# Optimization experiments

Hardware: AMD Instinct MI355X
Metric: run time of the kernel (lower is better)

Reference implementation:

```python
import jax, jax.numpy as jnp
import numpy as np
import math

EPS = 1.1920929e-07  # torch F.rms_norm default eps = fp32 machine epsilon


def rms_norm(x):
    # normalize over last dim, no learned weight (matches F.rms_norm(x, (d,)))
    var = jnp.mean(jnp.square(x), axis=-1, keepdims=True)
    return x * jax.lax.rsqrt(var + EPS)


def rotary(x, cos, sin):
    # x: (B, T, H, D); cos/sin: (T, D) -> broadcast over B, H
    d2 = x.shape[-1] // 2
    x1, x2 = x[..., :d2], x[..., d2:]
    rot = jnp.concatenate([-x2, x1], axis=-1)  # rotate_half
    c = cos[None, :, None, :]
    s = sin[None, :, None, :]
    return x * c + rot * s


def setup_inputs() -> dict:
    key = jax.random.key(0)
    ks = jax.random.split(key, 5)
    B, T, C, H = 2, 2048, 1024, 16
    D = C // H
    x = jax.random.normal(ks[0], (B, T, C), dtype=jnp.float32)
    # real RoPE tables (theta=10000), duplicated across the two halves
    inv_freq = 1.0 / (10000.0 ** (np.arange(0, D, 2, dtype=np.float32) / D))
    pos = np.arange(T, dtype=np.float32)
    freqs = np.outer(pos, inv_freq)            # (T, D/2)
    emb = np.concatenate([freqs, freqs], -1)   # (T, D)
    cos = jnp.asarray(np.cos(emb), dtype=jnp.float32)
    sin = jnp.asarray(np.sin(emb), dtype=jnp.float32)
    sc_in = 1.0 / math.sqrt(C)
    W_attn = jax.random.normal(ks[1], (C, 3 * C), dtype=jnp.float32) * sc_in
    b_attn = jax.random.normal(ks[2], (3 * C,), dtype=jnp.float32) * 0.02
    W_proj = jax.random.normal(ks[3], (C, C), dtype=jnp.float32) * sc_in
    b_proj = jax.random.normal(ks[4], (C,), dtype=jnp.float32) * 0.02
    return {"x": x, "cos": cos, "sin": sin, "W_attn": W_attn, "b_attn": b_attn,
            "W_proj": W_proj, "b_proj": b_proj}


def reference(x, cos, sin, W_attn, b_attn, W_proj, b_proj):
    B, T, C = x.shape
    H = 16
    D = C // H
    qkv = x @ W_attn + b_attn                         # (B, T, 3C)
    qkv = qkv.reshape(B, T, 3, H, D)                  # 'b t (a h d) -> ...'
    q, k, v = qkv[:, :, 0], qkv[:, :, 1], qkv[:, :, 2]  # (B, T, H, D)
    q, k = rms_norm(q), rms_norm(k)
    q = rotary(q, cos, sin)
    k = rotary(k, cos, sin)
    # causal SDPA, scale = 1/sqrt(D)
    scale = 1.0 / math.sqrt(D)
    scores = jnp.einsum('bthd,bshd->bhts', q, k) * scale  # (B, H, T, T)
    causal = jnp.tril(jnp.ones((T, T), dtype=bool))
    scores = jnp.where(causal[None, None], scores, jnp.finfo(scores.dtype).min)
    attn = jax.nn.softmax(scores, axis=-1)
    y = jnp.einsum('bhts,bshd->bthd', attn, v)            # (B, T, H, D)
    y = y.reshape(B, T, C)
    return y @ W_proj + b_proj
```

## Files before the change

kernel.cpp:

```cpp
#include <hip/hip_runtime.h>
#include <math.h>

#define EPSV 1.1920929e-07f

typedef __attribute__((ext_vector_type(8))) short short8;
typedef __attribute__((ext_vector_type(4))) float f32x4;

__device__ __forceinline__ float bf2f(unsigned short u) {
    union { unsigned int i; float f; } c; c.i = ((unsigned int)u) << 16; return c.f;
}
__device__ __forceinline__ unsigned short f2bf(float f) {
    union { float f; unsigned int i; } c; c.f = f;
    unsigned int r = c.i + 0x7FFFu + ((c.i >> 16) & 1u);
    return (unsigned short)(r >> 16);
}
__device__ __forceinline__ unsigned int pack_bf16_ru(float a, float b) {
    union { float f; unsigned int i; } ca, cb; ca.f = a; cb.f = b;
    return __builtin_amdgcn_perm(cb.i + 0x8000u, ca.i + 0x8000u, 0x07060302u);
}
__device__ __forceinline__ void async_lds16(const unsigned short* g, unsigned short* l) {
    __builtin_amdgcn_global_load_lds(
        (const __attribute__((address_space(1))) unsigned int*)g,
        (__attribute__((address_space(3))) unsigned int*)l, 16, 0, 0);
}

__global__ __launch_bounds__(256) void prep_cast_transpose(
    const float* __restrict__ x, unsigned short* __restrict__ xb, int nCast,
    const float* __restrict__ Wa, unsigned short* __restrict__ Wat,
    const float* __restrict__ Wp, unsigned short* __restrict__ Wpt,
    int castBlocks)
{
    __shared__ float tile[32][33];
    const int bxg = blockIdx.x;
    if (bxg < castBlocks) {
        const int i = (bxg * 256 + threadIdx.x) * 4;
        if (i >= nCast) return;
        const float4 v = *(const float4*)&x[i];
        ushort4 o;
        o.x = f2bf(v.x); o.y = f2bf(v.y); o.z = f2bf(v.z); o.w = f2bf(v.w);
        *(ushort4*)&xb[i] = o;
        return;
    }
    const int r0 = bxg - castBlocks;
    int bx = r0 & 127;
    const int by = r0 >> 7;
    const float* W; unsigned short* Wt; int N;
    if (bx < 96) { W = Wa; Wt = Wat; N = 3072; }
    else         { W = Wp; Wt = Wpt; N = 1024; bx -= 96; }
    const int n0 = bx * 32, k0 = by * 32;
    const int r = threadIdx.x >> 3, c4 = (threadIdx.x & 7) * 4;
    const float4 v = *(const float4*)&W[(size_t)(k0 + r) * N + n0 + c4];
    tile[r][c4 + 0] = v.x; tile[r][c4 + 1] = v.y;
    tile[r][c4 + 2] = v.z; tile[r][c4 + 3] = v.w;
    __syncthreads();
    ushort4 o;
    o.x = f2bf(tile[c4 + 0][r]); o.y = f2bf(tile[c4 + 1][r]);
    o.z = f2bf(tile[c4 + 2][r]); o.w = f2bf(tile[c4 + 3][r]);
    *(ushort4*)&Wt[(size_t)(n0 + r) * 1024 + k0 + c4] = o;
}

template <bool OUT_BF16>
__global__ __launch_bounds__(256) void gemm_bf16(
    const unsigned short* __restrict__ A,
    const unsigned short* __restrict__ Bt,
    const float* __restrict__ bias,
    void* __restrict__ Cv,
    int M, int N, int K)
{
    __shared__ unsigned short As0[128][32], As1[128][32];
    __shared__ unsigned short Bs0[128][32], Bs1[128][32];
    const int t    = threadIdx.x;
    const int lane = t & 63;
    const int wv   = t >> 6;
    const int wrow = (wv >> 1) * 64;
    const int wcol = (wv & 1) * 64;
    const int m0 = blockIdx.y * 128;
    const int n0 = blockIdx.x * 128;
    const int col  = lane & 15;
    const int quad = lane >> 4;

    const int srow = (wv << 5) + (lane >> 2);
    const int scol = (lane & 3) << 3;
    const unsigned short* a00 = A  + (size_t)(m0 + srow) * K + scol;
    const unsigned short* a10 = a00 + (size_t)16 * K;
    const unsigned short* a01 = a00 + 32;
    const unsigned short* a11 = a10 + 32;
    const unsigned short* b00 = Bt + (size_t)(n0 + srow) * K + scol;
    const unsigned short* b10 = b00 + (size_t)16 * K;
    const unsigned short* b01 = b00 + 32;
    const unsigned short* b11 = b10 + 32;
    unsigned short* al0 = &As0[srow][scol];
    unsigned short* al1 = &As0[srow + 16][scol];
    unsigned short* al2 = &As1[srow][scol];
    unsigned short* al3 = &As1[srow + 16][scol];
    unsigned short* bl0 = &Bs0[srow][scol];
    unsigned short* bl1 = &Bs0[srow + 16][scol];
    unsigned short* bl2 = &Bs1[srow][scol];
    unsigned short* bl3 = &Bs1[srow + 16][scol];

    f32x4 acc[4][4];
    #pragma unroll
    for (int i = 0; i < 4; ++i)
        #pragma unroll
        for (int j = 0; j < 4; ++j)
            acc[i][j] = (f32x4){0.f, 0.f, 0.f, 0.f};

    for (int k0 = 0; k0 < K; k0 += 64) {
        async_lds16(a00, al0);
        async_lds16(a10, al1);
        async_lds16(a01, al2);
        async_lds16(a11, al3);
        async_lds16(b00, bl0);
        async_lds16(b10, bl1);
        async_lds16(b01, bl2);
        async_lds16(b11, bl3);
        a00 += 64; a10 += 64; a01 += 64; a11 += 64;
        b00 += 64; b10 += 64; b01 += 64; b11 += 64;
        __syncthreads();
        short8 af[2][4], bf[2][4];
        #pragma unroll
        for (int mt = 0; mt < 4; ++mt) {
            af[0][mt] = *(const short8*)&As0[wrow + mt * 16 + col][quad << 3];
            af[1][mt] = *(const short8*)&As1[wrow + mt * 16 + col][quad << 3];
        }
        #pragma unroll
        for (int nt = 0; nt < 4; ++nt) {
            bf[0][nt] = *(const short8*)&Bs0[wcol + nt * 16 + col][quad << 3];
            bf[1][nt] = *(const short8*)&Bs1[wcol + nt * 16 + col][quad << 3];
        }
        #pragma unroll
        for (int ks = 0; ks < 2; ++ks)
            #pragma unroll
            for (int mt = 0; mt < 4; ++mt)
                #pragma unroll
                for (int nt = 0; nt < 4; ++nt)
                    acc[mt][nt] = __builtin_amdgcn_mfma_f32_16x16x32_bf16(
                        af[ks][mt], bf[ks][nt], acc[mt][nt], 0, 0, 0);
        __syncthreads();
    }

    const int rowq = quad << 2;
    #pragma unroll
    for (int nt = 0; nt < 4; ++nt) {
        const int n = n0 + wcol + nt * 16 + col;
        const float bv = bias[n];
        #pragma unroll
        for (int mt = 0; mt < 4; ++mt) {
            #pragma unroll
            for (int r = 0; r < 4; ++r) {
                const int m = m0 + wrow + mt * 16 + rowq + r;
                const float v = acc[mt][nt][r] + bv;
                if (OUT_BF16)
                    ((unsigned short*)Cv)[(size_t)m * N + n] = f2bf(v);
                else
                    ((float*)Cv)[(size_t)m * N + n] = v;
            }
        }
    }
}

__global__ __launch_bounds__(256) void gemm_bf16_n64(
    const unsigned short* __restrict__ A,
    const unsigned short* __restrict__ Bt,
    const float* __restrict__ bias,
    float* __restrict__ C,
    int M, int N, int K)
{
    __shared__ unsigned short As0[128][32], As1[128][32];
    __shared__ unsigned short Bs0[64][32], Bs1[64][32];
    const int t    = threadIdx.x;
    const int lane = t & 63;
    const int wv   = t >> 6;
    const int wrow = wv << 5;
    const int m0 = blockIdx.y * 128;
    const int n0 = blockIdx.x * 64;
    const int col  = lane & 15;
    const int quad = lane >> 4;

    const int srow = (wv << 5) + (lane >> 2);
    const int scol = (lane & 3) << 3;
    const unsigned short* a00 = A  + (size_t)(m0 + srow) * K + scol;
    const unsigned short* a10 = a00 + (size_t)16 * K;
    const unsigned short* a01 = a00 + 32;
    const unsigned short* a11 = a10 + 32;
    const int bsrow = (wv << 4) + (lane >> 2);
    const unsigned short* b00 = Bt + (size_t)(n0 + bsrow) * K + scol;
    const unsigned short* b01 = b00 + 32;
    unsigned short* al0 = &As0[srow][scol];
    unsigned short* al1 = &As0[srow + 16][scol];
    unsigned short* al2 = &As1[srow][scol];
    unsigned short* al3 = &As1[srow + 16][scol];
    unsigned short* bl0 = &Bs0[bsrow][scol];
    unsigned short* bl1 = &Bs1[bsrow][scol];

    f32x4 acc[2][4];
    #pragma unroll
    for (int i = 0; i < 2; ++i)
        #pragma unroll
        for (int j = 0; j < 4; ++j)
            acc[i][j] = (f32x4){0.f, 0.f, 0.f, 0.f};

    for (int k0 = 0; k0 < K; k0 += 64) {
        async_lds16(a00, al0);
        async_lds16(a10, al1);
        async_lds16(a01, al2);
        async_lds16(a11, al3);
        async_lds16(b00, bl0);
        async_lds16(b01, bl1);
        a00 += 64; a10 += 64; a01 += 64; a11 += 64;
        b00 += 64; b01 += 64;
        __syncthreads();
        short8 af[2][2], bf[2][4];
        #pragma unroll
        for (int mt = 0; mt < 2; ++mt) {
            af[0][mt] = *(const short8*)&As0[wrow + mt * 16 + col][quad << 3];
            af[1][mt] = *(const short8*)&As1[wrow + mt * 16 + col][quad << 3];
        }
        #pragma unroll
        for (int nt = 0; nt < 4; ++nt) {
            bf[0][nt] = *(const short8*)&Bs0[nt * 16 + col][quad << 3];
            bf[1][nt] = *(const short8*)&Bs1[nt * 16 + col][quad << 3];
        }
        #pragma unroll
        for (int ks = 0; ks < 2; ++ks)
            #pragma unroll
            for (int mt = 0; mt < 2; ++mt)
                #pragma unroll
                for (int nt = 0; nt < 4; ++nt)
                    acc[mt][nt] = __builtin_amdgcn_mfma_f32_16x16x32_bf16(
                        af[ks][mt], bf[ks][nt], acc[mt][nt], 0, 0, 0);
        __syncthreads();
    }

    const int rowq = quad << 2;
    #pragma unroll
    for (int nt = 0; nt < 4; ++nt) {
        const int n = n0 + nt * 16 + col;
        const float bv = bias[n];
        #pragma unroll
        for (int mt = 0; mt < 2; ++mt) {
            #pragma unroll
            for (int r = 0; r < 4; ++r) {
                const int m = m0 + wrow + mt * 16 + rowq + r;
                C[(size_t)m * N + n] = acc[mt][nt][r] + bv;
            }
        }
    }
}

__global__ __launch_bounds__(256) void rmsrope_vt(
    unsigned short* __restrict__ qkv, const float* __restrict__ cosp,
    const float* __restrict__ sinp, unsigned short* __restrict__ vt,
    int BT, int T)
{
    __shared__ unsigned short tile[64][72];
    const int nrms = BT * 2;
    const int bxg = (int)blockIdx.x;
    if (bxg < nrms) {
        const int wid  = (bxg << 2) + (threadIdx.x >> 6);
        const int lane = threadIdx.x & 63;
        const int hq = wid & 3;
        const int w  = (wid >> 2) & 1;
        const int bt = wid >> 3;
        if (bt >= BT) return;
        const int h  = (hq << 2) + (lane >> 4);
        const int d4 = (lane & 15) << 2;
        const int tpos = bt % T;
        const size_t idx = (size_t)bt * 3072 + (w << 10) + (h << 6) + d4;

        const ushort4 u = *(const ushort4*)&qkv[idx];
        const float x0 = bf2f(u.x), x1 = bf2f(u.y), x2 = bf2f(u.z), x3 = bf2f(u.w);
        float ss = x0 * x0 + x1 * x1 + x2 * x2 + x3 * x3;
        ss += __shfl_xor(ss, 1, 64);
        ss += __shfl_xor(ss, 2, 64);
        ss += __shfl_xor(ss, 4, 64);
        ss += __shfl_xor(ss, 8, 64);
        const float rn = rsqrtf(ss * (1.0f / 64.0f) + EPSV);
        const float xn0 = x0 * rn, xn1 = x1 * rn, xn2 = x2 * rn, xn3 = x3 * rn;
        const float p0 = __shfl_xor(xn0, 8, 64);
        const float p1 = __shfl_xor(xn1, 8, 64);
        const float p2 = __shfl_xor(xn2, 8, 64);
        const float p3 = __shfl_xor(xn3, 8, 64);
        const float sgn = (d4 < 32) ? -1.0f : 1.0f;
        const float4 c = *(const float4*)&cosp[tpos * 64 + d4];
        const float4 s = *(const float4*)&sinp[tpos * 64 + d4];
        const float scale = (w == 0) ? 0.18033688011112042f : 1.0f;
        ushort4 o;
        o.x = f2bf(fmaf(xn0, c.x, sgn * p0 * s.x) * scale);
        o.y = f2bf(fmaf(xn1, c.y, sgn * p1 * s.y) * scale);
        o.z = f2bf(fmaf(xn2, c.z, sgn * p2 * s.z) * scale);
        o.w = f2bf(fmaf(xn3, c.w, sgn * p3 * s.w) * scale);
        *(ushort4*)&qkv[idx] = o;
        return;
    }
    const int r0 = bxg - nrms;
    const int tdiv = T >> 6;
    const int bh = r0 / tdiv;
    const int ty = r0 - bh * tdiv;
    const int b  = bh >> 4, h = bh & 15;
    const int t0 = ty << 6;
    const int t  = threadIdx.x;
    const unsigned short* vbase = qkv + (size_t)b * T * 3072 + 2048 + (h << 6);

    #pragma unroll
    for (int i = 0; i < 2; ++i) {
        const int c = t + (i << 8);
        const int r = c >> 3, c8 = (c & 7) << 3;
        const short8 v = *(const short8*)&vbase[(size_t)(t0 + r) * 3072 + c8];
        #pragma unroll
        for (int j = 0; j < 8; ++j)
            tile[c8 + j][r] = (unsigned short)v[j];
    }
    __syncthreads();
    #pragma unroll
    for (int i = 0; i < 2; ++i) {
        const int c = t + (i << 8);
        const int d = c >> 3, c8 = (c & 7) << 3;
        const short8 o = *(const short8*)&tile[d][c8];
        *(short8*)&vt[((size_t)bh * 64 + d) * T + t0 + c8] = o;
    }
}

__global__ __launch_bounds__(512, 4) void flash_attn_mfma(
    const unsigned short* __restrict__ qkv,
    const unsigned short* __restrict__ vt,
    unsigned short* __restrict__ yb,
    int B, int T)
{
    const int bh = blockIdx.x;
    const int b  = bh >> 4, h = bh & 15;
    const int ny = (int)gridDim.y;
    const int y  = (int)blockIdx.y;
    const int hny = (ny + 1) >> 1;
    const int jq = (y < hny) ? (ny - 1 - y) : (y - hny);
    const int q0 = jq << 7;
    const int t  = threadIdx.x;
    const int lane = t & 63;
    const int w    = t >> 6;
    const int col  = lane & 15;
    const int quad = lane >> 4;

    __shared__ __align__(16) unsigned short smem[25600];
    unsigned short* Kb = smem;
    unsigned short* Vb = smem + 8192;
    unsigned short* Ps = smem + 16384;

    const unsigned short* qb  = qkv + (size_t)b * T * 3072 + (h << 6);
    const unsigned short* kb  = qb + 1024;
    const unsigned short* vtb = vt + (size_t)bh * 64 * T;

    const int qw = q0 + (w << 4);
    const int qg = qw + col;

    short8 qf[2];
    {
        const unsigned short* qrow = qb + (size_t)qg * 3072 + (quad << 3);
        qf[0] = *(const short8*)&qrow[0];
        qf[1] = *(const short8*)&qrow[32];
    }

    f32x4 oacc[4];
    #pragma unroll
    for (int i = 0; i < 4; ++i) oacc[i] = (f32x4){0.f, 0.f, 0.f, 0.f};
    float l_i = 0.f;

    const int sr = t >> 3;
    const int sg = (((t & 7) ^ (sr & 7)) << 3);
    const unsigned short* kp = kb  + (size_t)sr * 3072 + sg;
    const unsigned short* vp = vtb + (size_t)sr * T + sg;

    async_lds16(kp, Kb + (t << 3));
    async_lds16(vp, Vb + (t << 3));
    kp += (size_t)64 * 3072; vp += 64;

    const int cs0 = ((quad ^ (col & 7)) << 3);
    const int cs1 = (((4 + quad) ^ (col & 7)) << 3);

    const int last_kt = (q0 + 127) >> 6;
    int cur = 0;
    for (int kt = 0; kt <= last_kt; ++kt) {
        const int k0 = kt << 6;
        __syncthreads();
        if (kt < last_kt) {
            async_lds16(kp, Kb + ((cur ^ 1) << 12) + (t << 3));
            async_lds16(vp, Vb + ((cur ^ 1) << 12) + (t << 3));
            kp += (size_t)64 * 3072; vp += 64;
        }

        if (k0 <= qw + 15) {
            const unsigned short* Kc = Kb + (cur << 12);
            const unsigned short* Vc = Vb + (cur << 12);

            f32x4 st[4];
            #pragma unroll
            for (int i = 0; i < 4; ++i) st[i] = (f32x4){0.f, 0.f, 0.f, 0.f};
            __builtin_amdgcn_s_setprio(1);
            #pragma unroll
            for (int ks = 0; ks < 2; ++ks)
                #pragma unroll
                for (int mt = 0; mt < 4; ++mt) {
                    const short8 kf = *(const short8*)&Kc[(mt * 16 + col) * 64 + (ks ? cs1 : cs0)];
                    st[mt] = __builtin_amdgcn_mfma_f32_16x16x32_bf16(kf, qf[ks], st[mt], 0, 0, 0);
                }
            __builtin_amdgcn_s_setprio(0);

            const bool diag = (k0 + 63 > qw);
            unsigned short* pw = Ps + ((w << 4) + col) * 72;
            float rs = 0.f;
            #pragma unroll
            for (int mt = 0; mt < 4; ++mt) {
                float x0 = st[mt][0], x1 = st[mt][1];
                float x2 = st[mt][2], x3 = st[mt][3];
                if (diag) {
                    const int sbase = k0 + mt * 16 + (quad << 2);
                    if (sbase + 0 > qg) x0 = -INFINITY;
                    if (sbase + 1 > qg) x1 = -INFINITY;
                    if (sbase + 2 > qg) x2 = -INFINITY;
                    if (sbase + 3 > qg) x3 = -INFINITY;
                }
                const float p0 = __builtin_amdgcn_exp2f(x0);
                const float p1 = __builtin_amdgcn_exp2f(x1);
                const float p2 = __builtin_amdgcn_exp2f(x2);
                const float p3 = __builtin_amdgcn_exp2f(x3);
                rs += (p0 + p1) + (p2 + p3);
                uint2 pk;
                pk.x = pack_bf16_ru(p0, p1);
                pk.y = pack_bf16_ru(p2, p3);
                *(uint2*)&pw[mt * 16 + (quad << 2)] = pk;
            }
            l_i += rs;

            __builtin_amdgcn_s_setprio(1);
            #pragma unroll
            for (int ks = 0; ks < 2; ++ks) {
                const short8 pf = *(const short8*)&Ps[((w << 4) + col) * 72 + ks * 32 + (quad << 3)];
                #pragma unroll
                for (int mt = 0; mt < 4; ++mt) {
                    const short8 vf = *(const short8*)&Vc[(mt * 16 + col) * 64 + (ks ? cs1 : cs0)];
                    oacc[mt] = __builtin_amdgcn_mfma_f32_16x16x32_bf16(vf, pf, oacc[mt], 0, 0, 0);
                }
            }
            __builtin_amdgcn_s_setprio(0);
        }
        cur ^= 1;
    }

    l_i += __shfl_xor(l_i, 16, 64);
    l_i += __shfl_xor(l_i, 32, 64);
    const float inv = 1.0f / l_i;
    unsigned short* yrow = yb + (size_t)(b * T + qg) * 1024 + (h << 6);
    #pragma unroll
    for (int mt = 0; mt < 4; ++mt) {
        ushort4 yv;
        yv.x = f2bf(oacc[mt][0] * inv);
        yv.y = f2bf(oacc[mt][1] * inv);
        yv.z = f2bf(oacc[mt][2] * inv);
        yv.w = f2bf(oacc[mt][3] * inv);
        *(ushort4*)&yrow[mt * 16 + (quad << 2)] = yv;
    }
}

extern "C" void kernel_launch(void* const* d_in, const int* in_sizes, int n_in,
                              void* d_out, int out_size, void* d_ws, size_t ws_size,
                              hipStream_t stream)
{
    const float* x      = (const float*)d_in[0];
    const float* cosp   = (const float*)d_in[1];
    const float* sinp   = (const float*)d_in[2];
    const float* W_attn = (const float*)d_in[3];
    const float* b_attn = (const float*)d_in[4];
    const float* W_proj = (const float*)d_in[5];
    const float* b_proj = (const float*)d_in[6];
    float* out = (float*)d_out;

    const int C = 1024, H = 16;
    const int T  = in_sizes[1] / 64;
    const int BT = in_sizes[0] / C;
    const int B  = BT / T;

    unsigned short* qkvb = (unsigned short*)d_ws;
    unsigned short* xb   = qkvb + (size_t)BT * 3072;
    unsigned short* Wab  = xb   + (size_t)BT * 1024;
    unsigned short* Wpb  = Wab  + (size_t)3072 * 1024;
    unsigned short* yb   = Wpb  + (size_t)1024 * 1024;
    unsigned short* vtb  = xb;

    const int castBlocks = BT * C / 1024;
    prep_cast_transpose<<<dim3(castBlocks + 4096), dim3(256), 0, stream>>>(
        x, xb, BT * C, W_attn, Wab, W_proj, Wpb, castBlocks);

    gemm_bf16<true><<<dim3(3 * C / 128, BT / 128), dim3(256), 0, stream>>>(
        xb, Wab, b_attn, qkvb, BT, 3 * C, C);

    rmsrope_vt<<<dim3(BT * 2 + B * H * (T >> 6)), dim3(256), 0, stream>>>(
        qkvb, cosp, sinp, vtb, BT, T);

    flash_attn_mfma<<<dim3(B * H, T / 128), dim3(512), 0, stream>>>(
        qkvb, vtb, yb, B, T);

    gemm_bf16_n64<<<dim3(C / 64, BT / 128), dim3(256), 0, stream>>>(
        yb, Wpb, b_proj, out, BT, C, C);
}
```

Measured before the change: 186.2 us.

## Fuse RMSNorm, RoPE and V transpose into QKV GEMM epilogue

Removes the separate rmsrope_vt kernel. The QKV GEMM epilogue now computes the per-head RMS norm with wave shuffles, applies rotary using a packed cos/sin table built in the prep kernel, and writes V transposed through LDS. This removes one launch and a full bf16 round trip of q/k/v through global memory. In exchange the epilogue uses strided 2-byte stores, holds more registers, and adds an extra workspace buffer for vt.

```diff
diff --git a/kernel.cpp b/kernel.cpp
--- a/kernel.cpp
+++ b/kernel.cpp
@@ -28,7 +28,8 @@
     const float* __restrict__ x, unsigned short* __restrict__ xb, int nCast,
     const float* __restrict__ Wa, unsigned short* __restrict__ Wat,
     const float* __restrict__ Wp, unsigned short* __restrict__ Wpt,
-    int castBlocks)
+    const float* __restrict__ cosp, const float* __restrict__ sinp,
+    float2* __restrict__ cs, int castBlocks)
 {
     __shared__ float tile[32][33];
     const int bxg = blockIdx.x;
@@ -39,6 +40,12 @@
         ushort4 o;
         o.x = f2bf(v.x); o.y = f2bf(v.y); o.z = f2bf(v.z); o.w = f2bf(v.w);
         *(ushort4*)&xb[i] = o;
+        return;
+    }
+    if (bxg >= castBlocks + 4096) {
+        const int i = (bxg - castBlocks - 4096) * 256 + threadIdx.x;
+        const int tp = i >> 5, dp = i & 31;
+        cs[i] = make_float2(cosp[tp * 64 + dp], sinp[tp * 64 + dp]);
         return;
     }
     const int r0 = bxg - castBlocks;
@@ -59,16 +66,22 @@
     *(ushort4*)&Wt[(size_t)(n0 + r) * 1024 + k0 + c4] = o;
 }
 
-template <bool OUT_BF16>
-__global__ __launch_bounds__(256) void gemm_bf16(
+__global__ __launch_bounds__(256) void gemm_qkv(
     const unsigned short* __restrict__ A,
     const unsigned short* __restrict__ Bt,
     const float* __restrict__ bias,
-    void* __restrict__ Cv,
-    int M, int N, int K)
+    unsigned short* __restrict__ qkv,
+    unsigned short* __restrict__ vt,
+    const float2* __restrict__ cs,
+    int M, int K, int T)
 {
-    __shared__ unsigned short As0[128][32], As1[128][32];
-    __shared__ unsigned short Bs0[128][32], Bs1[128][32];
+    const int N = 3072;
+    __shared__ __align__(16) unsigned short smem[17408];
+    unsigned short* As0 = smem;
+    unsigned short* As1 = smem + 4096;
+    unsigned short* Bs0 = smem + 8192;
+    unsigned short* Bs1 = smem + 12288;
+
     const int t    = threadIdx.x;
     const int lane = t & 63;
     const int wv   = t >> 6;
@@ -89,14 +102,14 @@
     const unsigned short* b10 = b00 + (size_t)16 * K;
     const unsigned short* b01 = b00 + 32;
     const unsigned short* b11 = b10 + 32;
-    unsigned short* al0 = &As0[srow][scol];
-    unsigned short* al1 = &As0[srow + 16][scol];
-    unsigned short* al2 = &As1[srow][scol];
-    unsigned short* al3 = &As1[srow + 16][scol];
-    unsigned short* bl0 = &Bs0[srow][scol];
-    unsigned short* bl1 = &Bs0[srow + 16][scol];
-    unsigned short* bl2 = &Bs1[srow][scol];
-    unsigned short* bl3 = &Bs1[srow + 16][scol];
+    unsigned short* al0 = &As0[srow * 32 + scol];
+    unsigned short* al1 = &As0[(srow + 16) * 32 + scol];
+    unsigned short* al2 = &As1[srow * 32 + scol];
+    unsigned short* al3 = &As1[(srow + 16) * 32 + scol];
+    unsigned short* bl0 = &Bs0[srow * 32 + scol];
+    unsigned short* bl1 = &Bs0[(srow + 16) * 32 + scol];
+    unsigned short* bl2 = &Bs1[srow * 32 + scol];
+    unsigned short* bl3 = &Bs1[(srow + 16) * 32 + scol];
 
     f32x4 acc[4][4];
     #pragma unroll
@@ -120,13 +133,13 @@
         short8 af[2][4], bf[2][4];
         #pragma unroll
         for (int mt = 0; mt < 4; ++mt) {
-            af[0][mt] = *(const short8*)&As0[wrow + mt * 16 + col][quad << 3];
-            af[1][mt] = *(const short8*)&As1[wrow + mt * 16 + col][quad << 3];
+            af[0][mt] = *(const short8*)&As0[(wrow + mt * 16 + col) * 32 + (quad << 3)];
+            af[1][mt] = *(const short8*)&As1[(wrow + mt * 16 + col) * 32 + (quad << 3)];
         }
         #pragma unroll
         for (int nt = 0; nt < 4; ++nt) {
-            bf[0][nt] = *(const short8*)&Bs0[wcol + nt * 16 + col][quad << 3];
-            bf[1][nt] = *(const short8*)&Bs1[wcol + nt * 16 + col][quad << 3];
+            bf[0][nt] = *(const short8*)&Bs0[(wcol + nt * 16 + col) * 32 + (quad << 3)];
+            bf[1][nt] = *(const short8*)&Bs1[(wcol + nt * 16 + col) * 32 + (quad << 3)];
         }
         #pragma unroll
         for (int ks = 0; ks < 2; ++ks)
@@ -139,22 +152,72 @@
         __syncthreads();
     }
 
-    const int rowq = quad << 2;
     #pragma unroll
     for (int nt = 0; nt < 4; ++nt) {
-        const int n = n0 + wcol + nt * 16 + col;
-        const float bv = bias[n];
+        const float bv = bias[n0 + wcol + nt * 16 + col];
+        #pragma unroll
+        for (int mt = 0; mt < 4; ++mt)
+            #pragma unroll
+            for (int r = 0; r < 4; ++r)
+                acc[mt][nt][r] += bv;
+    }
+
+    const int b     = m0 / T;
+    const int tpos0 = m0 - b * T;
+
+    if (n0 < 2048) {
+        const int n_lin = n0 + wcol;
+        const float scale = (n_lin < 1024) ? 0.18033688011112042f : 1.0f;
         #pragma unroll
         for (int mt = 0; mt < 4; ++mt) {
             #pragma unroll
             for (int r = 0; r < 4; ++r) {
-                const int m = m0 + wrow + mt * 16 + rowq + r;
-                const float v = acc[mt][nt][r] + bv;
-                if (OUT_BF16)
-                    ((unsigned short*)Cv)[(size_t)m * N + n] = f2bf(v);
-                else
-                    ((float*)Cv)[(size_t)m * N + n] = v;
+                float ss = acc[mt][0][r] * acc[mt][0][r]
+                         + acc[mt][1][r] * acc[mt][1][r]
+                         + acc[mt][2][r] * acc[mt][2][r]
+                         + acc[mt][3][r] * acc[mt][3][r];
+                ss += __shfl_xor(ss, 1, 64);
+                ss += __shfl_xor(ss, 2, 64);
+                ss += __shfl_xor(ss, 4, 64);
+                ss += __shfl_xor(ss, 8, 64);
+                const float rn = rsqrtf(ss * (1.0f / 64.0f) + EPSV) * scale;
+                const int tpos = tpos0 + wrow + mt * 16 + (quad << 2) + r;
+                const float2 c0 = cs[tpos * 32 + col];
+                const float2 c1 = cs[tpos * 32 + 16 + col];
+                const float o0 = (acc[mt][0][r] * c0.x - acc[mt][2][r] * c0.y) * rn;
+                const float o1 = (acc[mt][1][r] * c1.x - acc[mt][3][r] * c1.y) * rn;
+                const float o2 = (acc[mt][2][r] * c0.x + acc[mt][0][r] * c0.y) * rn;
+                const float o3 = (acc[mt][3][r] * c1.x + acc[mt][1][r] * c1.y) * rn;
+                const int m = m0 + wrow + mt * 16 + (quad << 2) + r;
+                unsigned short* qr = qkv + (size_t)m * N + n_lin + col;
+                qr[0]  = f2bf(o0);
+                qr[16] = f2bf(o1);
+                qr[32] = f2bf(o2);
+                qr[48] = f2bf(o3);
             }
+        }
+    } else {
+        unsigned short (*vtile)[136] = (unsigned short(*)[136])smem;
+        __syncthreads();
+        #pragma unroll
+        for (int nt = 0; nt < 4; ++nt)
+            #pragma unroll
+            for (int mt = 0; mt < 4; ++mt)
+                #pragma unroll
+                for (int r = 0; r < 4; ++r)
+                    vtile[wcol + nt * 16 + col][wrow + mt * 16 + (quad << 2) + r]
+                        = f2bf(acc[mt][nt][r]);
+        __syncthreads();
+        const int td = t >> 4;
+        const int mloc = (t & 15) << 3;
+        const int h2base = (n0 - 2048) >> 6;
+        #pragma unroll
+        for (int i = 0; i < 8; ++i) {
+            const int dl = td + i * 16;
+            const short8 o = *(const short8*)&vtile[dl][mloc];
+            const int h2 = h2base + (dl >> 6);
+            const size_t row = ((size_t)(b * 16 + h2) << 6) + (dl & 63);
+            *(short8*)&vt[row * T + tpos0 + mloc] = o;
         }
     }
 }
@@ -245,79 +308,6 @@
                 C[(size_t)m * N + n] = acc[mt][nt][r] + bv;
             }
         }
-    }
-}
-
-__global__ __launch_bounds__(256) void rmsrope_vt(
-    unsigned short* __restrict__ qkv, const float* __restrict__ cosp,
-    const float* __restrict__ sinp, unsigned short* __restrict__ vt,
-    int BT, int T)
-{
-    __shared__ unsigned short tile[64][72];
-    const int nrms = BT * 2;
-    const int bxg = (int)blockIdx.x;
-    if (bxg < nrms) {
-        const int wid  = (bxg << 2) + (threadIdx.x >> 6);
-        const int lane = threadIdx.x & 63;
-        const int hq = wid & 3;
-        const int w  = (wid >> 2) & 1;
-        const int bt = wid >> 3;
-        if (bt >= BT) return;
-        const int h  = (hq << 2) + (lane >> 4);
-        const int d4 = (lane & 15) << 2;
-        const int tpos = bt % T;
-        const size_t idx = (size_t)bt * 3072 + (w << 10) + (h << 6) + d4;
-
-        const ushort4 u = *(const ushort4*)&qkv[idx];
-        const float x0 = bf2f(u.x), x1 = bf2f(u.y), x2 = bf2f(u.z), x3 = bf2f(u.w);
-        float ss = x0 * x0 + x1 * x1 + x2 * x2 + x3 * x3;
-        ss += __shfl_xor(ss, 1, 64);
-        ss += __shfl_xor(ss, 2, 64);
-        ss += __shfl_xor(ss, 4, 64);
-        ss += __shfl_xor(ss, 8, 64);
-        const float rn = rsqrtf(ss * (1.0f / 64.0f) + EPSV);
-        const float xn0 = x0 * rn, xn1 = x1 * rn, xn2 = x2 * rn, xn3 = x3 * rn;
-        const float p0 = __shfl_xor(xn0, 8, 64);
-        const float p1 = __shfl_xor(xn1, 8, 64);
-        const float p2 = __shfl_xor(xn2, 8, 64);
-        const float p3 = __shfl_xor(xn3, 8, 64);
-        const float sgn = (d4 < 32) ? -1.0f : 1.0f;
-        const float4 c = *(const float4*)&cosp[tpos * 64 + d4];
-        const float4 s = *(const float4*)&sinp[tpos * 64 + d4];
-        const float scale = (w == 0) ? 0.18033688011112042f : 1.0f;
-        ushort4 o;
-        o.x = f2bf(fmaf(xn0, c.x, sgn * p0 * s.x) * scale);
-        o.y = f2bf(fmaf(xn1, c.y, sgn * p1 * s.y) * scale);
-        o.z = f2bf(fmaf(xn2, c.z, sgn * p2 * s.z) * scale);
-        o.w = f2bf(fmaf(xn3, c.w, sgn * p3 * s.w) * scale);
-        *(ushort4*)&qkv[idx] = o;
-        return;
-    }
-    const int r0 = bxg - nrms;
-    const int tdiv = T >> 6;
-    const int bh = r0 / tdiv;
-    const int ty = r0 - bh * tdiv;
-    const int b  = bh >> 4, h = bh & 15;
-    const int t0 = ty << 6;
-    const int t  = threadIdx.x;
-    const unsigned short* vbase = qkv + (size_t)b * T * 3072 + 2048 + (h << 6);
-
-    #pragma unroll
-    for (int i = 0; i < 2; ++i) {
-        const int c = t + (i << 8);
-        const int r = c >> 3, c8 = (c & 7) << 3;
-        const short8 v = *(const short8*)&vbase[(size_t)(t0 + r) * 3072 + c8];
-        #pragma unroll
-        for (int j = 0; j < 8; ++j)
-            tile[c8 + j][r] = (unsigned short)v[j];
-    }
-    __syncthreads();
-    #pragma unroll
-    for (int i = 0; i < 2; ++i) {
-        const int c = t + (i << 8);
-        const int d = c >> 3, c8 = (c & 7) << 3;
-        const short8 o = *(const short8*)&tile[d][c8];
-        *(short8*)&vt[((size_t)bh * 64 + d) * T + t0 + c8] = o;
     }
 }
 
@@ -478,22 +468,21 @@
     const int BT = in_sizes[0] / C;
     const int B  = BT / T;
 
-    unsigned short* qkvb = (unsigned short*)d_ws;
+    float2* csb          = (float2*)d_ws;
+    unsigned short* qkvb = (unsigned short*)(csb + (size_t)T * 32);
     unsigned short* xb   = qkvb + (size_t)BT * 3072;
     unsigned short* Wab  = xb   + (size_t)BT * 1024;
     unsigned short* Wpb  = Wab  + (size_t)3072 * 1024;
     unsigned short* yb   = Wpb  + (size_t)1024 * 1024;
-    unsigned short* vtb  = xb;
+    unsigned short* vtb  = yb   + (size_t)BT * 1024;
 
     const int castBlocks = BT * C / 1024;
-    prep_cast_transpose<<<dim3(castBlocks + 4096), dim3(256), 0, stream>>>(
-        x, xb, BT * C, W_attn, Wab, W_proj, Wpb, castBlocks);
-
-    gemm_bf16<true><<<dim3(3 * C / 128, BT / 128), dim3(256), 0, stream>>>(
-        xb, Wab, b_attn, qkvb, BT, 3 * C, C);
-
-    rmsrope_vt<<<dim3(BT * 2 + B * H * (T >> 6)), dim3(256), 0, stream>>>(
-        qkvb, cosp, sinp, vtb, BT, T);
+    const int csBlocks   = T * 32 / 256;
+    prep_cast_transpose<<<dim3(castBlocks + 4096 + csBlocks), dim3(256), 0, stream>>>(
+        x, xb, BT * C, W_attn, Wab, W_proj, Wpb, cosp, sinp, csb, castBlocks);
+
+    gemm_qkv<<<dim3(3 * C / 128, BT / 128), dim3(256), 0, stream>>>(
+        xb, Wab, b_attn, qkvb, vtb, csb, BT, C, T);
 
     flash_attn_mfma<<<dim3(B * H, T / 128), dim3(512), 0, stream>>>(
         qkvb, vtb, yb, B, T);
```

Result: faster. 176.9 us (-5.0%).
